# Kernel tuning notes

Hardware: AMD Instinct MI355X
Metric: run time of the kernel (lower is better)

The kernel has to match this reference:

```python
import jax, jax.numpy as jnp
import numpy as np

NUM_GRAPHS = 8
N_NODES = 50000
N_EDGES = 800000
F_IN = 128
HID = 256
EPS_BN = 1e-5


def _gat(x, ei, W, a_src, a_dst, b, heads, out_dim):
    # PyG GATConv: h = x @ W -> [N, heads, out]; edge (j=src -> i=dst)
    N = x.shape[0]
    h = (x @ W).reshape(N, heads, out_dim)
    alpha_src = jnp.sum(h * a_src, axis=-1)  # [N, H]
    alpha_dst = jnp.sum(h * a_dst, axis=-1)  # [N, H]
    src, dst = ei[0], ei[1]
    e = jax.nn.leaky_relu(alpha_src[src] + alpha_dst[dst], 0.2)  # [E, H]
    # segment softmax over edges grouped by destination node
    m = jax.ops.segment_max(e, dst, num_segments=N)
    m = jnp.where(jnp.isfinite(m), m, 0.0)
    ex = jnp.exp(e - m[dst])
    denom = jax.ops.segment_sum(ex, dst, num_segments=N)
    alpha = ex / (denom[dst] + 1e-16)
    msg = h[src] * alpha[:, :, None]  # [E, H, out]
    agg = jax.ops.segment_sum(msg, dst, num_segments=N)
    return agg.reshape(N, heads * out_dim) + b


def _bn(h, gamma, beta):
    # BatchNorm over nodes (training-mode batch statistics, biased variance)
    mu = h.mean(axis=0)
    var = h.var(axis=0)
    return gamma * (h - mu) / jnp.sqrt(var + EPS_BN) + beta


def setup_inputs() -> dict:
    key = jax.random.key(0)
    ks = jax.random.split(key, 16)
    s = 0.05
    inp = {
        "x": jax.random.normal(ks[0], (N_NODES, F_IN), dtype=jnp.float32),
        "edge_index": jax.random.randint(ks[1], (2, N_EDGES), 0, N_NODES, dtype=jnp.int64) if False else jax.random.randint(ks[1], (2, N_EDGES), 0, N_NODES),
        "batch_index": jnp.sort(jax.random.randint(ks[2], (N_NODES,), 0, NUM_GRAPHS)),
        # conv1: GATConv(128, 64, heads=4)
        "W1": jax.random.normal(ks[3], (F_IN, HID), dtype=jnp.float32) * s,
        "a_src1": jax.random.normal(ks[4], (4, 64), dtype=jnp.float32) * s,
        "a_dst1": jax.random.normal(ks[5], (4, 64), dtype=jnp.float32) * s,
        "b1": jnp.zeros((HID,), jnp.float32),
        "g1": jnp.ones((HID,), jnp.float32),
        "beta1": jnp.zeros((HID,), jnp.float32),
        # conv2: GATConv(256, 256, heads=1)
        "W2": jax.random.normal(ks[6], (HID, HID), dtype=jnp.float32) * s,
        "a_src2": jax.random.normal(ks[7], (1, HID), dtype=jnp.float32) * s,
        "a_dst2": jax.random.normal(ks[8], (1, HID), dtype=jnp.float32) * s,
        "b2": jnp.zeros((HID,), jnp.float32),
        "g2": jnp.ones((HID,), jnp.float32),
        "beta2": jnp.zeros((HID,), jnp.float32),
        # q_head: Linear(512,256) -> ReLU -> Linear(256,4)
        "Wq1": jax.random.normal(ks[9], (2 * HID, HID), dtype=jnp.float32) * s,
        "bq1": jnp.zeros((HID,), jnp.float32),
        "Wq2": jax.random.normal(ks[10], (HID, 4), dtype=jnp.float32) * s,
        "bq2": jnp.zeros((4,), jnp.float32),
    }
    return inp


def reference(x, edge_index, batch_index, W1, a_src1, a_dst1, b1, g1, beta1,
              W2, a_src2, a_dst2, b2, g2, beta2, Wq1, bq1, Wq2, bq2):
    N = x.shape[0]
    loops = jnp.arange(N, dtype=edge_index.dtype)
    ei = jnp.concatenate([edge_index, jnp.stack([loops, loops])], axis=1)
    h = jax.nn.relu(_bn(_gat(x, ei, W1, a_src1, a_dst1, b1, 4, 64), g1, beta1))
    h = jax.nn.relu(_bn(_gat(h, ei, W2, a_src2, a_dst2, b2, 1, HID), g2, beta2))
    sums = jax.ops.segment_sum(h, batch_index, num_segments=NUM_GRAPHS)
    cnt = jax.ops.segment_sum(jnp.ones((N, 1), h.dtype), batch_index, num_segments=NUM_GRAPHS)
    gmean = sums / jnp.maximum(cnt, 1.0)
    ctx = jnp.concatenate([h, gmean[batch_index]], axis=1)  # [N, 512]
    q = jax.nn.relu(ctx @ Wq1 + bq1) @ Wq2 + bq2  # [N, 4]
    return (q, batch_index)
```

## Files before the change

### kernel.cpp

```cpp
#include <hip/hip_runtime.h>
#include <hip/hip_bf16.h>
#include <math.h>

#define F_IN  128
#define HIDC  256
#define NG    8
#define EPS_BN 1e-5f

typedef unsigned short u16;
typedef unsigned int   u32;
typedef unsigned char  u8;
typedef __attribute__((ext_vector_type(8))) short bf16x8;
typedef __attribute__((ext_vector_type(4))) float f32x4;
typedef __attribute__((ext_vector_type(2))) float f32x2;

static __device__ __forceinline__ float b2f(u16 u) {
    return __uint_as_float((u32)u << 16);
}
static __device__ __forceinline__ u16 f2b(float f) {
    u32 u = __float_as_uint(f);
    u32 r = (u + 0x7fffu + ((u >> 16) & 1u)) >> 16;
    return (u16)r;
}
static __device__ __forceinline__ u32 pack2(float a, float b) {
    return (u32)f2b(a) | ((u32)f2b(b) << 16);
}
static __device__ __forceinline__ float lk(float v) {
    return v >= 0.f ? v : 0.2f * v;
}
static __device__ __forceinline__ u8 f2fp8(float v) {
    return (u8)__builtin_amdgcn_cvt_pk_fp8_f32(v, v, 0, false);
}

__global__ void prep_kernel(const float* __restrict__ x,
                            const float* __restrict__ W1,
                            const float* __restrict__ W2,
                            const float* __restrict__ Wq1,
                            u32* __restrict__ xb, u16* __restrict__ WT1,
                            u16* __restrict__ WT2, u16* __restrict__ WQT,
                            int npair) {
    int i = blockIdx.x * 256 + threadIdx.x;
    if (i < npair) {
        float2 v = ((const float2*)x)[i];
        xb[i] = pack2(v.x, v.y);
        return;
    }
    i -= npair;
    if (i < F_IN * HIDC) {
        int nn = i / F_IN, k = i % F_IN;
        WT1[i] = f2b(W1[(long)k * HIDC + nn]);
        return;
    }
    i -= F_IN * HIDC;
    if (i < HIDC * HIDC) {
        int nn = i / HIDC, k = i % HIDC;
        WT2[i] = f2b(W2[(long)k * HIDC + nn]);
        return;
    }
    i -= HIDC * HIDC;
    if (i < HIDC * HIDC) {
        int nn = i / HIDC, k = i % HIDC;
        WQT[i] = f2b(Wq1[(long)k * HIDC + nn]);
    }
}

__global__ void out_init_kernel(float* __restrict__ out,
                                const float* __restrict__ bq2,
                                const int* __restrict__ batch, int N) {
    int i = blockIdx.x * 256 + threadIdx.x;
    if (i < N * 4) out[i] = bq2[i & 3];
    else if (i < N * 5) out[i] = (float)batch[i - N * 4];
}

__global__ void bn_coef_kernel(const float* __restrict__ sum,
                               const float* __restrict__ sumsq,
                               const float* __restrict__ gamma,
                               const float* __restrict__ beta,
                               float* __restrict__ scale,
                               float* __restrict__ bias, int N) {
    int c = threadIdx.x;
    float invN = 1.f / (float)N;
    float mu = sum[c] * invN;
    float var = sumsq[c] * invN - mu * mu;
    float inv = rsqrtf(var + EPS_BN);
    float sc = gamma[c] * inv;
    scale[c] = sc;
    bias[c] = beta[c] - mu * sc;
}

template <int K, int MODE>
__global__ __launch_bounds__(256)
void gemm_mfma_kernel(const u16* __restrict__ A, const u16* __restrict__ WT,
                      u8* __restrict__ C, int M,
                      const float* __restrict__ scaleA, const float* __restrict__ biasA,
                      const float* __restrict__ wsrc, const float* __restrict__ wdst,
                      float* __restrict__ asrc, float* __restrict__ adst,
                      const float* __restrict__ gproj, const int* __restrict__ bat,
                      const float* __restrict__ bq1,
                      const float* __restrict__ wq2, float* __restrict__ qout) {
    constexpr int BK = 128;
    constexpr int ROWCH = BK / 8;
    __shared__ u16 sB[64][BK + 8];
    int tid = threadIdx.x;
    int n0 = blockIdx.x * 64;

    int wid = tid >> 6, lane = tid & 63;
    int row = lane & 15, quad = lane >> 4;
    int m0 = blockIdx.y * 128 + wid * 32;
    int mf0 = m0, mf1 = m0 + 16;
    bool v0 = mf0 < M, v1 = mf1 < M;
    int mr0 = v0 ? mf0 : 0, mr1 = v1 ? mf1 : 0;
    const u16* Ap0 = A + (size_t)(mr0 + row) * K + quad * 8;
    const u16* Ap1 = A + (size_t)(mr1 + row) * K + quad * 8;

    f32x4 acc[2][4];
#pragma unroll
    for (int f = 0; f < 2; ++f)
#pragma unroll
        for (int t = 0; t < 4; ++t) acc[f][t] = (f32x4){0.f, 0.f, 0.f, 0.f};

#pragma unroll
    for (int kt = 0; kt < K; kt += BK) {
        if (kt > 0) __syncthreads();
        for (int i = tid; i < 64 * ROWCH; i += 256) {
            int r = i / ROWCH, c = i % ROWCH;
            *(uint4*)&sB[r][c * 8] =
                *(const uint4*)(WT + (size_t)(n0 + r) * K + kt + c * 8);
        }
        __syncthreads();
#pragma unroll
        for (int kk = 0; kk < BK; kk += 32) {
            int k0 = kt + kk;
            bf16x8 a[2];
            a[0] = *(const bf16x8*)(Ap0 + k0);
            a[1] = *(const bf16x8*)(Ap1 + k0);
            if constexpr (MODE != 0) {
                int c0 = k0 + quad * 8;
                float4 s0 = *(const float4*)(scaleA + c0);
                float4 s1 = *(const float4*)(scaleA + c0 + 4);
                float4 b0 = *(const float4*)(biasA + c0);
                float4 b1 = *(const float4*)(biasA + c0 + 4);
#pragma unroll
                for (int f = 0; f < 2; ++f) {
                    float xv[8];
#pragma unroll
                    for (int j = 0; j < 8; ++j) xv[j] = b2f((u16)a[f][j]);
                    xv[0] = fmaxf(fmaf(s0.x, xv[0], b0.x), 0.f);
                    xv[1] = fmaxf(fmaf(s0.y, xv[1], b0.y), 0.f);
                    xv[2] = fmaxf(fmaf(s0.z, xv[2], b0.z), 0.f);
                    xv[3] = fmaxf(fmaf(s0.w, xv[3], b0.w), 0.f);
                    xv[4] = fmaxf(fmaf(s1.x, xv[4], b1.x), 0.f);
                    xv[5] = fmaxf(fmaf(s1.y, xv[5], b1.y), 0.f);
                    xv[6] = fmaxf(fmaf(s1.z, xv[6], b1.z), 0.f);
                    xv[7] = fmaxf(fmaf(s1.w, xv[7], b1.w), 0.f);
#pragma unroll
                    for (int j = 0; j < 8; ++j) a[f][j] = (short)f2b(xv[j]);
                }
            }
#pragma unroll
            for (int t = 0; t < 4; ++t) {
                bf16x8 b = *(const bf16x8*)&sB[t * 16 + row][kk + quad * 8];
                acc[0][t] = __builtin_amdgcn_mfma_f32_16x16x32_bf16(a[0], b, acc[0][t], 0, 0, 0);
                acc[1][t] = __builtin_amdgcn_mfma_f32_16x16x32_bf16(a[1], b, acc[1][t], 0, 0, 0);
            }
        }
    }

    int mf[2] = {mf0, mf1};
    bool vf[2] = {v0, v1};
    if constexpr (MODE == 2) {
        float qacc[2][4][4];
#pragma unroll
        for (int f = 0; f < 2; ++f)
#pragma unroll
            for (int r = 0; r < 4; ++r)
#pragma unroll
                for (int j = 0; j < 4; ++j) qacc[f][r][j] = 0.f;
#pragma unroll
        for (int f = 0; f < 2; ++f) {
            if (!vf[f]) continue;
            int bm[4];
#pragma unroll
            for (int r = 0; r < 4; ++r) bm[r] = bat[mf[f] + quad * 4 + r];
#pragma unroll
            for (int t = 0; t < 4; ++t) {
                int n = n0 + t * 16 + row;
                float bq = bq1[n];
                float4 w4 = ((const float4*)wq2)[n];
#pragma unroll
                for (int r = 0; r < 4; ++r) {
                    float v = fmaxf(acc[f][t][r] + gproj[bm[r] * HIDC + n] + bq, 0.f);
                    qacc[f][r][0] = fmaf(v, w4.x, qacc[f][r][0]);
                    qacc[f][r][1] = fmaf(v, w4.y, qacc[f][r][1]);
                    qacc[f][r][2] = fmaf(v, w4.z, qacc[f][r][2]);
                    qacc[f][r][3] = fmaf(v, w4.w, qacc[f][r][3]);
                }
            }
        }
#pragma unroll
        for (int off = 1; off < 16; off <<= 1)
#pragma unroll
            for (int f = 0; f < 2; ++f)
#pragma unroll
                for (int r = 0; r < 4; ++r)
#pragma unroll
                    for (int j = 0; j < 4; ++j)
                        qacc[f][r][j] += __shfl_xor(qacc[f][r][j], off, 64);
        if (row == 0) {
#pragma unroll
            for (int f = 0; f < 2; ++f) {
                if (!vf[f]) continue;
#pragma unroll
                for (int r = 0; r < 4; ++r) {
                    size_t m = mf[f] + quad * 4 + r;
#pragma unroll
                    for (int j = 0; j < 4; ++j)
                        atomicAdd(&qout[m * 4 + j], qacc[f][r][j]);
                }
            }
        }
    } else {
#pragma unroll
        for (int f = 0; f < 2; ++f) {
            if (!vf[f]) continue;
#pragma unroll
            for (int t = 0; t < 4; ++t) {
                int n = n0 + t * 16 + row;
#pragma unroll
                for (int r = 0; r < 4; ++r)
                    C[(size_t)(mf[f] + quad * 4 + r) * HIDC + n] = f2fp8(acc[f][t][r]);
            }
        }
        if constexpr (MODE == 0) {
            float pa[2][4] = {}, pd[2][4] = {};
#pragma unroll
            for (int t = 0; t < 4; ++t) {
                float ws = wsrc[n0 + t * 16 + row];
                float wd = wdst[n0 + t * 16 + row];
#pragma unroll
                for (int f = 0; f < 2; ++f)
#pragma unroll
                    for (int r = 0; r < 4; ++r) {
                        pa[f][r] = fmaf(acc[f][t][r], ws, pa[f][r]);
                        pd[f][r] = fmaf(acc[f][t][r], wd, pd[f][r]);
                    }
            }
#pragma unroll
            for (int off = 1; off < 16; off <<= 1)
#pragma unroll
                for (int f = 0; f < 2; ++f)
#pragma unroll
                    for (int r = 0; r < 4; ++r) {
                        pa[f][r] += __shfl_xor(pa[f][r], off, 64);
                        pd[f][r] += __shfl_xor(pd[f][r], off, 64);
                    }
            if (row == 0) {
                int hb = n0 >> 6;
#pragma unroll
                for (int f = 0; f < 2; ++f) {
                    if (!vf[f]) continue;
#pragma unroll
                    for (int r = 0; r < 4; ++r) {
                        int m = mf[f] + quad * 4 + r;
                        asrc[m * 4 + hb] = pa[f][r];
                        adst[m * 4 + hb] = pd[f][r];
                    }
                }
            }
        }
        if constexpr (MODE == 1) {
            float pa[2][4] = {}, pd[2][4] = {};
#pragma unroll
            for (int t = 0; t < 4; ++t) {
                float ws = wsrc[n0 + t * 16 + row];
                float wd = wdst[n0 + t * 16 + row];
#pragma unroll
                for (int f = 0; f < 2; ++f)
#pragma unroll
                    for (int r = 0; r < 4; ++r) {
                        pa[f][r] = fmaf(acc[f][t][r], ws, pa[f][r]);
                        pd[f][r] = fmaf(acc[f][t][r], wd, pd[f][r]);
                    }
            }
#pragma unroll
            for (int off = 1; off < 16; off <<= 1)
#pragma unroll
                for (int f = 0; f < 2; ++f)
#pragma unroll
                    for (int r = 0; r < 4; ++r) {
                        pa[f][r] += __shfl_xor(pa[f][r], off, 64);
                        pd[f][r] += __shfl_xor(pd[f][r], off, 64);
                    }
            if (row == 0) {
#pragma unroll
                for (int f = 0; f < 2; ++f) {
                    if (!vf[f]) continue;
#pragma unroll
                    for (int r = 0; r < 4; ++r) {
                        int m = mf[f] + quad * 4 + r;
                        atomicAdd(&asrc[m], pa[f][r]);
                        atomicAdd(&adst[m], pd[f][r]);
                    }
                }
            }
        }
    }
}

__global__ void deg_kernel(const int* __restrict__ ei, int E, int N,
                           int* __restrict__ deg) {
    int e = blockIdx.x * blockDim.x + threadIdx.x;
    if (e >= E + N) return;
    int d = (e < E) ? ei[E + e] : (e - E);
    atomicAdd(&deg[d], 1);
}

__global__ __launch_bounds__(256)
void scan_phase1(const int* __restrict__ deg, int* __restrict__ part,
                 int* __restrict__ bsum, int N) {
    __shared__ int tmp[256];
    int i = blockIdx.x * 256 + threadIdx.x;
    int v = (i < N) ? deg[i] : 0;
    tmp[threadIdx.x] = v;
    __syncthreads();
    for (int off = 1; off < 256; off <<= 1) {
        int t = (threadIdx.x >= off) ? tmp[threadIdx.x - off] : 0;
        __syncthreads();
        tmp[threadIdx.x] += t;
        __syncthreads();
    }
    if (i < N) part[i] = tmp[threadIdx.x];
    if (threadIdx.x == 255) bsum[blockIdx.x] = tmp[255];
}
__global__ __launch_bounds__(256)
void scan_phase2(int* __restrict__ bsum, int nb) {
    __shared__ int tmp[256];
    int v = (threadIdx.x < nb) ? bsum[threadIdx.x] : 0;
    tmp[threadIdx.x] = v;
    __syncthreads();
    for (int off = 1; off < 256; off <<= 1) {
        int t = (threadIdx.x >= off) ? tmp[threadIdx.x - off] : 0;
        __syncthreads();
        tmp[threadIdx.x] += t;
        __syncthreads();
    }
    if (threadIdx.x < nb)
        bsum[threadIdx.x] = threadIdx.x ? tmp[threadIdx.x - 1] : 0;
}
__global__ __launch_bounds__(256)
void scan_phase3(const int* __restrict__ part, const int* __restrict__ bsum,
                 int* __restrict__ rowptr, int N) {
    int i = blockIdx.x * 256 + threadIdx.x;
    if (i < N) rowptr[i + 1] = part[i] + bsum[blockIdx.x];
    if (i == 0) rowptr[0] = 0;
}

__global__ void fill_kernel(const int* __restrict__ ei, int E, int N,
                            const int* __restrict__ rowptr,
                            int* __restrict__ cur, int* __restrict__ csr_src) {
    int e = blockIdx.x * blockDim.x + threadIdx.x;
    if (e >= E + N) return;
    int s = (e < E) ? ei[e] : (e - E);
    int d = (e < E) ? ei[E + e] : (e - E);
    int pos = rowptr[d] + atomicAdd(&cur[d], 1);
    csr_src[pos] = s;
}

template <int H>
__global__ __launch_bounds__(256)
void gat_gather_kernel(const int* __restrict__ rowptr,
                       const int* __restrict__ csr_src,
                       const float* __restrict__ asrc,
                       const float* __restrict__ adst,
                       const u8* __restrict__ h,
                       u16* __restrict__ agg, int N) {
    __shared__ __align__(16) uint2 s_ed[4][64 * H];
    int wid = threadIdx.x >> 6, lane = threadIdx.x & 63;
    int n = blockIdx.x * 4 + wid;
    if (n >= N) return;
    int start = rowptr[n], end = rowptr[n + 1];
    int deg = end - start;
    float ad[H];
#pragma unroll
    for (int hh = 0; hh < H; ++hh) ad[hh] = adst[n * H + hh];

    f32x2 acc01 = {0.f, 0.f}, acc23 = {0.f, 0.f};
    const int head = (H == 4) ? (lane >> 4) : 0;
    const u8* hb = h;
    const u32 laneB = (u32)lane * 4u;
    float wsum[H];

#define GBODY(J) {                                                             \
            uint2 e_ = s_ed[wid][(H == 4) ? ((J) * 4 + head) : (J)];           \
            u32 hv_ = *(const u32*)(hb + (size_t)(e_.x + laneB));              \
            float al_ = __uint_as_float(e_.y);                                 \
            f32x2 al2_ = {al_, al_};                                           \
            f32x2 v01_ = __builtin_amdgcn_cvt_pk_f32_fp8(hv_, false);          \
            f32x2 v23_ = __builtin_amdgcn_cvt_pk_f32_fp8(hv_, true);           \
            acc01 = __builtin_elementwise_fma(v01_, al2_, acc01);              \
            acc23 = __builtin_elementwise_fma(v23_, al2_, acc23); }

    if (deg <= 64) {
        float v[H];
#pragma unroll
        for (int hh = 0; hh < H; ++hh) v[hh] = -1e30f;
        u32 off = 0;
        if (lane < deg) {
            int s = csr_src[start + lane];
            off = (u32)s * (u32)HIDC;
            if (H == 4) {
                float4 a4 = *(const float4*)(asrc + s * 4);
                v[0] = lk(a4.x + ad[0]);
                v[1 % H] = lk(a4.y + ad[1 % H]);
                v[2 % H] = lk(a4.z + ad[2 % H]);
                v[3 % H] = lk(a4.w + ad[3 % H]);
            } else {
                v[0] = lk(asrc[s] + ad[0]);
            }
        }
        float m[H];
#pragma unroll
        for (int hh = 0; hh < H; ++hh) m[hh] = v[hh];
#pragma unroll
        for (int o = 1; o < 64; o <<= 1)
#pragma unroll
            for (int hh = 0; hh < H; ++hh)
                m[hh] = fmaxf(m[hh], __shfl_xor(m[hh], o, 64));
        float w[H];
#pragma unroll
        for (int hh = 0; hh < H; ++hh) {
            w[hh] = __expf(v[hh] - m[hh]);
            wsum[hh] = w[hh];
        }
#pragma unroll
        for (int o = 1; o < 64; o <<= 1)
#pragma unroll
            for (int hh = 0; hh < H; ++hh)
                wsum[hh] += __shfl_xor(wsum[hh], o, 64);
        if (H == 4) {
            uint4 w0, w1;
            w0.x = off; w0.y = __float_as_uint(w[0]);
            w0.z = off; w0.w = __float_as_uint(w[1 % H]);
            w1.x = off; w1.y = __float_as_uint(w[2 % H]);
            w1.z = off; w1.w = __float_as_uint(w[3 % H]);
            *(uint4*)&s_ed[wid][lane * 4] = w0;
            *(uint4*)&s_ed[wid][lane * 4 + 2] = w1;
        } else {
            s_ed[wid][lane] = make_uint2(off, __float_as_uint(w[0]));
        }
        int j = 0;
        for (; j + 4 <= deg; j += 4) { GBODY(j) GBODY(j + 1) GBODY(j + 2) GBODY(j + 3) }
        for (; j < deg; ++j) GBODY(j)
    } else {
        float m[H];
#pragma unroll
        for (int hh = 0; hh < H; ++hh) m[hh] = -1e30f;
        for (int i = start + lane; i < end; i += 64) {
            int s = csr_src[i];
            if (H == 4) {
                float4 a4 = *(const float4*)(asrc + s * 4);
                m[0] = fmaxf(m[0], lk(a4.x + ad[0]));
                m[1 % H] = fmaxf(m[1 % H], lk(a4.y + ad[1 % H]));
                m[2 % H] = fmaxf(m[2 % H], lk(a4.z + ad[2 % H]));
                m[3 % H] = fmaxf(m[3 % H], lk(a4.w + ad[3 % H]));
            } else {
                m[0] = fmaxf(m[0], lk(asrc[s] + ad[0]));
            }
        }
#pragma unroll
        for (int o = 1; o < 64; o <<= 1)
#pragma unroll
            for (int hh = 0; hh < H; ++hh)
                m[hh] = fmaxf(m[hh], __shfl_xor(m[hh], o, 64));
#pragma unroll
        for (int hh = 0; hh < H; ++hh) wsum[hh] = 0.f;
        for (int base = start; base < end; base += 64) {
            int cnt = min(64, end - base);
            if (lane < cnt) {
                int s = csr_src[base + lane];
                u32 off = (u32)s * (u32)HIDC;
                if (H == 4) {
                    float4 a4 = *(const float4*)(asrc + s * 4);
                    float w0f = __expf(lk(a4.x + ad[0]) - m[0]);
                    float w1f = __expf(lk(a4.y + ad[1 % H]) - m[1 % H]);
                    float w2f = __expf(lk(a4.z + ad[2 % H]) - m[2 % H]);
                    float w3f = __expf(lk(a4.w + ad[3 % H]) - m[3 % H]);
                    wsum[0] += w0f; wsum[1 % H] += w1f;
                    wsum[2 % H] += w2f; wsum[3 % H] += w3f;
                    uint4 w0, w1;
                    w0.x = off; w0.y = __float_as_uint(w0f);
                    w0.z = off; w0.w = __float_as_uint(w1f);
                    w1.x = off; w1.y = __float_as_uint(w2f);
                    w1.z = off; w1.w = __float_as_uint(w3f);
                    *(uint4*)&s_ed[wid][lane * 4] = w0;
                    *(uint4*)&s_ed[wid][lane * 4 + 2] = w1;
                } else {
                    float wf = __expf(lk(asrc[s] + ad[0]) - m[0]);
                    wsum[0] += wf;
                    s_ed[wid][lane] = make_uint2(off, __float_as_uint(wf));
                }
            }
            int j = 0;
            for (; j + 4 <= cnt; j += 4) { GBODY(j) GBODY(j + 1) GBODY(j + 2) GBODY(j + 3) }
            for (; j < cnt; ++j) GBODY(j)
        }
#pragma unroll
        for (int o = 1; o < 64; o <<= 1)
#pragma unroll
            for (int hh = 0; hh < H; ++hh)
                wsum[hh] += __shfl_xor(wsum[hh], o, 64);
    }
#undef GBODY
    float sc = 1.f / (wsum[head] + 1e-16f);
    f32x2 sc2 = {sc, sc};
    acc01 *= sc2;
    acc23 *= sc2;
    uint2 o;
    o.x = pack2(acc01.x, acc01.y);
    o.y = pack2(acc23.x, acc23.y);
    ((uint2*)(agg + (size_t)n * HIDC))[lane] = o;
}

__global__ __launch_bounds__(256)
void bn_stats_kernel(const u16* __restrict__ h, int N,
                     float* __restrict__ sum, float* __restrict__ sumsq) {
    int c = threadIdx.x;
    int r0 = blockIdx.x * 128;
    int rend = min(r0 + 128, N);
    float s = 0.f, q = 0.f;
    for (int r = r0; r < rend; ++r) {
        float v = b2f(h[(long)r * HIDC + c]);
        s += v;
        q += v * v;
    }
    atomicAdd(&sum[c], s);
    atomicAdd(&sumsq[c], q);
}

__global__ __launch_bounds__(256)
void pool_bn_kernel(const u16* __restrict__ h, const int* __restrict__ batch,
                    int N, const float* __restrict__ scale,
                    const float* __restrict__ bias,
                    float* __restrict__ gsum, float* __restrict__ gcnt) {
    int c = threadIdx.x;
    float sc = scale[c], bi = bias[c];
    int r0 = blockIdx.x * 128;
    int rend = min(r0 + 128, N);
    int curb = -1;
    float acc = 0.f;
    for (int r = r0; r < rend; ++r) {
        int b = batch[r];
        if (b != curb) {
            if (curb >= 0) atomicAdd(&gsum[curb * HIDC + c], acc);
            curb = b; acc = 0.f;
        }
        acc += fmaxf(fmaf(sc, b2f(h[(long)r * HIDC + c]), bi), 0.f);
    }
    if (curb >= 0) atomicAdd(&gsum[curb * HIDC + c], acc);
    if (c == 0) {
        int prev = -1; float cnt = 0.f;
        for (int r = r0; r < rend; ++r) {
            int b = batch[r];
            if (b != prev) {
                if (prev >= 0) atomicAdd(&gcnt[prev], cnt);
                prev = b; cnt = 0.f;
            }
            cnt += 1.f;
        }
        if (prev >= 0) atomicAdd(&gcnt[prev], cnt);
    }
}

__global__ __launch_bounds__(256)
void gmean_gproj_kernel(const float* __restrict__ gsum,
                        const float* __restrict__ gcnt,
                        const float* __restrict__ Wq1,
                        float* __restrict__ gproj) {
    int b = blockIdx.x, c = threadIdx.x;
    __shared__ float gm[HIDC];
    gm[c] = gsum[b * HIDC + c] / fmaxf(gcnt[b], 1.f);
    __syncthreads();
    float acc = 0.f;
    for (int k = 0; k < HIDC; ++k)
        acc = fmaf(gm[k], Wq1[(long)(HIDC + k) * HIDC + c], acc);
    gproj[b * HIDC + c] = acc;
}

extern "C" void kernel_launch(void* const* d_in, const int* in_sizes, int n_in,
                              void* d_out, int out_size, void* d_ws, size_t ws_size,
                              hipStream_t stream) {
    const float* x   = (const float*)d_in[0];
    const int*   ei  = (const int*)d_in[1];
    const int*   bat = (const int*)d_in[2];
    const float* W1  = (const float*)d_in[3];
    const float* as1 = (const float*)d_in[4];
    const float* ad1 = (const float*)d_in[5];
    const float* g1  = (const float*)d_in[7];
    const float* be1 = (const float*)d_in[8];
    const float* W2  = (const float*)d_in[9];
    const float* as2 = (const float*)d_in[10];
    const float* ad2 = (const float*)d_in[11];
    const float* g2  = (const float*)d_in[13];
    const float* be2 = (const float*)d_in[14];
    const float* Wq1 = (const float*)d_in[15];
    const float* bq1 = (const float*)d_in[16];
    const float* Wq2 = (const float*)d_in[17];
    const float* bq2 = (const float*)d_in[18];
    float* out = (float*)d_out;

    const int N = in_sizes[0] / F_IN;
    const int E = in_sizes[1] / 2;
    const int Etot = E + N;
    const int nb = (N + 255) / 256;

    const size_t hbytes = (size_t)N * HIDC * sizeof(u16);
    char* p = (char*)d_ws;
    auto alloc = [&](size_t sz) { char* q = p; p += (sz + 255) & ~(size_t)255; return q; };
    u16* BX   = (u16*)alloc((size_t)N * F_IN * sizeof(u16));
    u8*  BH   = (u8*)alloc((size_t)N * HIDC);
    u16* BA   = (u16*)alloc(hbytes);
    u16* WT1  = (u16*)alloc((size_t)HIDC * F_IN * sizeof(u16));
    u16* WT2  = (u16*)alloc((size_t)HIDC * HIDC * sizeof(u16));
    u16* WQT  = (u16*)alloc((size_t)HIDC * HIDC * sizeof(u16));
    float* asrc = (float*)alloc((size_t)N * 4 * 4 * 2);
    float* adst = asrc + (size_t)N * 4;
    int* rowptr  = (int*)alloc((size_t)(N + 1) * 4);
    int* csr_src = (int*)alloc((size_t)Etot * 4);
    int* cur     = (int*)alloc((size_t)N * 4 * 2);
    int* cur2    = cur + N;
    int* part    = (int*)alloc((size_t)N * 4);
    int* bsum    = (int*)alloc((size_t)nb * 4);
    float* bnsum = (float*)alloc(HIDC * 4 * 2);
    float* bnsq  = bnsum + HIDC;
    float* sc1   = (float*)alloc(HIDC * 4);
    float* bi1   = (float*)alloc(HIDC * 4);
    float* sc2   = (float*)alloc(HIDC * 4);
    float* bi2   = (float*)alloc(HIDC * 4);
    float* gsum  = (float*)alloc((NG * HIDC + NG) * 4);
    float* gcnt  = gsum + NG * HIDC;
    float* gproj = (float*)alloc(NG * HIDC * 4);

    dim3 gemmGrid(4, (N + 127) / 128);
    int edgeBlocks = (Etot + 255) / 256;
    int nodeBlocksW = (N + 3) / 4;
    int npair = N * F_IN / 2;
    int prepTotal = npair + F_IN * HIDC + 2 * HIDC * HIDC;

    hipMemsetAsync(cur, 0, (size_t)N * 4 * 2, stream);
    deg_kernel<<<edgeBlocks, 256, 0, stream>>>(ei, E, N, cur);
    scan_phase1<<<nb, 256, 0, stream>>>(cur, part, bsum, N);
    scan_phase2<<<1, 256, 0, stream>>>(bsum, nb);
    scan_phase3<<<nb, 256, 0, stream>>>(part, bsum, rowptr, N);
    fill_kernel<<<edgeBlocks, 256, 0, stream>>>(ei, E, N, rowptr, cur2, csr_src);

    prep_kernel<<<(prepTotal + 255) / 256, 256, 0, stream>>>(
        x, W1, W2, Wq1, (u32*)BX, WT1, WT2, WQT, npair);

    gemm_mfma_kernel<F_IN, 0><<<gemmGrid, 256, 0, stream>>>(
        BX, WT1, BH, N, nullptr, nullptr, as1, ad1, asrc, adst,
        nullptr, nullptr, nullptr, nullptr, nullptr);
    gat_gather_kernel<4><<<nodeBlocksW, 256, 0, stream>>>(rowptr, csr_src, asrc, adst, BH, BA, N);
    hipMemsetAsync(bnsum, 0, HIDC * 4 * 2, stream);
    bn_stats_kernel<<<(N + 127) / 128, 256, 0, stream>>>(BA, N, bnsum, bnsq);
    bn_coef_kernel<<<1, HIDC, 0, stream>>>(bnsum, bnsq, g1, be1, sc1, bi1, N);

    hipMemsetAsync(asrc, 0, (size_t)N * 4 * 4 * 2, stream);
    gemm_mfma_kernel<HIDC, 1><<<gemmGrid, 256, 0, stream>>>(
        BA, WT2, BH, N, sc1, bi1, as2, ad2, asrc, adst,
        nullptr, nullptr, nullptr, nullptr, nullptr);
    gat_gather_kernel<1><<<nodeBlocksW, 256, 0, stream>>>(rowptr, csr_src, asrc, adst, BH, BA, N);
    hipMemsetAsync(bnsum, 0, HIDC * 4 * 2, stream);
    bn_stats_kernel<<<(N + 127) / 128, 256, 0, stream>>>(BA, N, bnsum, bnsq);
    bn_coef_kernel<<<1, HIDC, 0, stream>>>(bnsum, bnsq, g2, be2, sc2, bi2, N);

    hipMemsetAsync(gsum, 0, (NG * HIDC + NG) * 4, stream);
    pool_bn_kernel<<<(N + 127) / 128, 256, 0, stream>>>(BA, bat, N, sc2, bi2, gsum, gcnt);
    gmean_gproj_kernel<<<NG, HIDC, 0, stream>>>(gsum, gcnt, Wq1, gproj);
    out_init_kernel<<<(N * 5 + 255) / 256, 256, 0, stream>>>(out, bq2, bat, N);

    gemm_mfma_kernel<HIDC, 2><<<gemmGrid, 256, 0, stream>>>(
        BA, WQT, nullptr, N, sc2, bi2, nullptr, nullptr, nullptr, nullptr,
        gproj, bat, bq1, Wq2, out);
}
```

Before: 544.0 us.

## Pre-swizzle weights into MFMA fragment order and tile GEMM by rows

The weight matrices are now written out during prep in MFMA B-fragment order, so each lane reads its bf16x8 operand straight from global memory with no LDS staging. The GEMM grid is reorganised so each block handles 32 rows across all 256 output columns, with each wave covering 64 columns. The A tile is loaded once into LDS and shared by the four waves, so activations are read once per row block instead of once for each of the four column blocks. The cost is that every block streams the whole weight matrix from global memory or cache, and the grid now has more, smaller blocks.

```diff
diff --git a/kernel.cpp b/kernel.cpp
--- a/kernel.cpp
+++ b/kernel.cpp
@@ -30,6 +30,19 @@
 }
 static __device__ __forceinline__ u8 f2fp8(float v) {
     return (u8)__builtin_amdgcn_cvt_pk_fp8_f32(v, v, 0, false);
+}
+
+static __device__ __forceinline__ u16 frag_elem(const float* __restrict__ W,
+                                                int i, int K) {
+    int j = i & 7;
+    int lane = (i >> 3) & 63;
+    int rest = i >> 9;
+    int ksteps = K >> 5;
+    int kst = rest % ksteps;
+    int ntile = rest / ksteps;
+    int k = kst * 32 + (lane >> 4) * 8 + j;
+    int n = ntile * 16 + (lane & 15);
+    return f2b(W[(long)k * HIDC + n]);
 }
 
 __global__ void prep_kernel(const float* __restrict__ x,
@@ -46,22 +59,11 @@
         return;
     }
     i -= npair;
-    if (i < F_IN * HIDC) {
-        int nn = i / F_IN, k = i % F_IN;
-        WT1[i] = f2b(W1[(long)k * HIDC + nn]);
-        return;
-    }
+    if (i < F_IN * HIDC) { WT1[i] = frag_elem(W1, i, F_IN); return; }
     i -= F_IN * HIDC;
-    if (i < HIDC * HIDC) {
-        int nn = i / HIDC, k = i % HIDC;
-        WT2[i] = f2b(W2[(long)k * HIDC + nn]);
-        return;
-    }
+    if (i < HIDC * HIDC) { WT2[i] = frag_elem(W2, i, HIDC); return; }
     i -= HIDC * HIDC;
-    if (i < HIDC * HIDC) {
-        int nn = i / HIDC, k = i % HIDC;
-        WQT[i] = f2b(Wq1[(long)k * HIDC + nn]);
-    }
+    if (i < HIDC * HIDC) { WQT[i] = frag_elem(Wq1, i, HIDC); }
 }
 
 __global__ void out_init_kernel(float* __restrict__ out,
@@ -90,7 +92,7 @@
 
 template <int K, int MODE>
 __global__ __launch_bounds__(256)
-void gemm_mfma_kernel(const u16* __restrict__ A, const u16* __restrict__ WT,
+void gemm_mfma_kernel(const u16* __restrict__ A, const u16* __restrict__ WTf,
                       u8* __restrict__ C, int M,
                       const float* __restrict__ scaleA, const float* __restrict__ biasA,
                       const float* __restrict__ wsrc, const float* __restrict__ wdst,
@@ -98,20 +100,24 @@
                       const float* __restrict__ gproj, const int* __restrict__ bat,
                       const float* __restrict__ bq1,
                       const float* __restrict__ wq2, float* __restrict__ qout) {
-    constexpr int BK = 128;
-    constexpr int ROWCH = BK / 8;
-    __shared__ u16 sB[64][BK + 8];
+    constexpr int KSTEPS = K / 32;
+    constexpr int RCH = K / 8;
+    __shared__ u16 sA[32][K + 8];
     int tid = threadIdx.x;
-    int n0 = blockIdx.x * 64;
+    int m0 = blockIdx.x * 32;
+
+    for (int i = tid; i < 32 * RCH; i += 256) {
+        int r = i / RCH, c = i % RCH;
+        int gm = m0 + r;
+        gm = gm < M ? gm : M - 1;
+        *(uint4*)&sA[r][c * 8] = *(const uint4*)(A + (size_t)gm * K + c * 8);
+    }
+    __syncthreads();
 
     int wid = tid >> 6, lane = tid & 63;
     int row = lane & 15, quad = lane >> 4;
-    int m0 = blockIdx.y * 128 + wid * 32;
     int mf0 = m0, mf1 = m0 + 16;
-    bool v0 = mf0 < M, v1 = mf1 < M;
-    int mr0 = v0 ? mf0 : 0, mr1 = v1 ? mf1 : 0;
-    const u16* Ap0 = A + (size_t)(mr0 + row) * K + quad * 8;
-    const u16* Ap1 = A + (size_t)(mr1 + row) * K + quad * 8;
+    bool v1 = mf1 < M;
 
     f32x4 acc[2][4];
 #pragma unroll
@@ -119,55 +125,48 @@
 #pragma unroll
         for (int t = 0; t < 4; ++t) acc[f][t] = (f32x4){0.f, 0.f, 0.f, 0.f};
 
-#pragma unroll
-    for (int kt = 0; kt < K; kt += BK) {
-        if (kt > 0) __syncthreads();
-        for (int i = tid; i < 64 * ROWCH; i += 256) {
-            int r = i / ROWCH, c = i % ROWCH;
-            *(uint4*)&sB[r][c * 8] =
-                *(const uint4*)(WT + (size_t)(n0 + r) * K + kt + c * 8);
-        }
-        __syncthreads();
-#pragma unroll
-        for (int kk = 0; kk < BK; kk += 32) {
-            int k0 = kt + kk;
-            bf16x8 a[2];
-            a[0] = *(const bf16x8*)(Ap0 + k0);
-            a[1] = *(const bf16x8*)(Ap1 + k0);
-            if constexpr (MODE != 0) {
-                int c0 = k0 + quad * 8;
-                float4 s0 = *(const float4*)(scaleA + c0);
-                float4 s1 = *(const float4*)(scaleA + c0 + 4);
-                float4 b0 = *(const float4*)(biasA + c0);
-                float4 b1 = *(const float4*)(biasA + c0 + 4);
-#pragma unroll
-                for (int f = 0; f < 2; ++f) {
-                    float xv[8];
-#pragma unroll
-                    for (int j = 0; j < 8; ++j) xv[j] = b2f((u16)a[f][j]);
-                    xv[0] = fmaxf(fmaf(s0.x, xv[0], b0.x), 0.f);
-                    xv[1] = fmaxf(fmaf(s0.y, xv[1], b0.y), 0.f);
-                    xv[2] = fmaxf(fmaf(s0.z, xv[2], b0.z), 0.f);
-                    xv[3] = fmaxf(fmaf(s0.w, xv[3], b0.w), 0.f);
-                    xv[4] = fmaxf(fmaf(s1.x, xv[4], b1.x), 0.f);
-                    xv[5] = fmaxf(fmaf(s1.y, xv[5], b1.y), 0.f);
-                    xv[6] = fmaxf(fmaf(s1.z, xv[6], b1.z), 0.f);
-                    xv[7] = fmaxf(fmaf(s1.w, xv[7], b1.w), 0.f);
-#pragma unroll
-                    for (int j = 0; j < 8; ++j) a[f][j] = (short)f2b(xv[j]);
-                }
-            }
-#pragma unroll
-            for (int t = 0; t < 4; ++t) {
-                bf16x8 b = *(const bf16x8*)&sB[t * 16 + row][kk + quad * 8];
-                acc[0][t] = __builtin_amdgcn_mfma_f32_16x16x32_bf16(a[0], b, acc[0][t], 0, 0, 0);
-                acc[1][t] = __builtin_amdgcn_mfma_f32_16x16x32_bf16(a[1], b, acc[1][t], 0, 0, 0);
-            }
-        }
-    }
-
+    const u16* Bbase = WTf + ((size_t)(wid * 4) * KSTEPS * 64 + lane) * 8;
+
+#pragma unroll
+    for (int ks = 0; ks < KSTEPS; ++ks) {
+        int kk = ks * 32 + quad * 8;
+        bf16x8 a[2];
+        a[0] = *(const bf16x8*)&sA[row][kk];
+        a[1] = *(const bf16x8*)&sA[16 + row][kk];
+        if constexpr (MODE != 0) {
+            int c0 = kk;
+            float4 s0 = *(const float4*)(scaleA + c0);
+            float4 s1 = *(const float4*)(scaleA + c0 + 4);
+            float4 b0 = *(const float4*)(biasA + c0);
+            float4 b1 = *(const float4*)(biasA + c0 + 4);
+#pragma unroll
+            for (int f = 0; f < 2; ++f) {
+                float xv[8];
+#pragma unroll
+                for (int j = 0; j < 8; ++j) xv[j] = b2f((u16)a[f][j]);
+                xv[0] = fmaxf(fmaf(s0.x, xv[0], b0.x), 0.f);
+                xv[1] = fmaxf(fmaf(s0.y, xv[1], b0.y), 0.f);
+                xv[2] = fmaxf(fmaf(s0.z, xv[2], b0.z), 0.f);
+                xv[3] = fmaxf(fmaf(s0.w, xv[3], b0.w), 0.f);
+                xv[4] = fmaxf(fmaf(s1.x, xv[4], b1.x), 0.f);
+                xv[5] = fmaxf(fmaf(s1.y, xv[5], b1.y), 0.f);
+                xv[6] = fmaxf(fmaf(s1.z, xv[6], b1.z), 0.f);
+                xv[7] = fmaxf(fmaf(s1.w, xv[7], b1.w), 0.f);
+#pragma unroll
+                for (int j = 0; j < 8; ++j) a[f][j] = (short)f2b(xv[j]);
+            }
+        }
+#pragma unroll
+        for (int t = 0; t < 4; ++t) {
+            bf16x8 b = *(const bf16x8*)(Bbase + ((size_t)t * KSTEPS + ks) * 512);
+            acc[0][t] = __builtin_amdgcn_mfma_f32_16x16x32_bf16(a[0], b, acc[0][t], 0, 0, 0);
+            acc[1][t] = __builtin_amdgcn_mfma_f32_16x16x32_bf16(a[1], b, acc[1][t], 0, 0, 0);
+        }
+    }
+
+    int n0 = wid * 64;
     int mf[2] = {mf0, mf1};
-    bool vf[2] = {v0, v1};
+    bool vf[2] = {true, v1};
     if constexpr (MODE == 2) {
         float qacc[2][4][4];
 #pragma unroll
@@ -255,15 +254,14 @@
                         pd[f][r] += __shfl_xor(pd[f][r], off, 64);
                     }
             if (row == 0) {
-                int hb = n0 >> 6;
 #pragma unroll
                 for (int f = 0; f < 2; ++f) {
                     if (!vf[f]) continue;
 #pragma unroll
                     for (int r = 0; r < 4; ++r) {
                         int m = mf[f] + quad * 4 + r;
-                        asrc[m * 4 + hb] = pa[f][r];
-                        adst[m * 4 + hb] = pd[f][r];
+                        asrc[m * 4 + wid] = pa[f][r];
+                        adst[m * 4 + wid] = pd[f][r];
                     }
                 }
             }
@@ -640,7 +638,7 @@
     float* gcnt  = gsum + NG * HIDC;
     float* gproj = (float*)alloc(NG * HIDC * 4);
 
-    dim3 gemmGrid(4, (N + 127) / 128);
+    dim3 gemmGrid((N + 31) / 32);
     int edgeBlocks = (Etot + 255) / 256;
     int nodeBlocksW = (N + 3) / 4;
     int npair = N * F_IN / 2;
```

Result: faster. 531.5 us (-2.3%).
